# Optimization experiments

Hardware: AMD Instinct MI355X
Metric: run time of the kernel (lower is better)

## Reference

```python
import jax, jax.numpy as jnp
import numpy as np

B, L, H, NH, T, WIN = 4, 4096, 256, 8, 64, 16
D = H // NH
NEG_SLOPE = 5.0
MASK_FILL = -1e12


def _leaky(x):
    return jnp.where(x >= 0, x, NEG_SLOPE * x)


def _window_indices():
    # static numpy index construction, mirrors EdgeBlock.self_attn
    off_u = np.concatenate([np.zeros(WIN + 1, np.int64), np.arange(1, WIN + 1)])
    off_d = np.concatenate([np.arange(-WIN, 0), np.zeros(WIN + 1, np.int64)])
    idx_u = np.arange(L)[:, None] + off_u  # [L, 2W+1]
    idx_d = np.arange(L)[:, None] + off_d  # [L, 2W+1]
    idx_mask = (idx_d >= 0) & (idx_u < L)
    return idx_u % L, idx_d % L, idx_mask


def setup_inputs() -> dict:
    key = jax.random.key(0)
    ks = jax.random.split(key, 12)
    s = 1.0 / np.sqrt(H)
    lengths = jnp.array([L, L - 128, L - 512, L - 1024])
    context_mask = jnp.arange(L)[None, :] < lengths[:, None]  # [B, L] bool
    return {
        'context': jax.random.normal(ks[0], (B, L, H), jnp.float32),
        'types': jax.random.normal(ks[1], (B, T, H), jnp.float32),
        'context_mask': context_mask,
        'W_types': jax.random.normal(ks[2], (H, H), jnp.float32) * s,
        'b_types': jnp.zeros((H,), jnp.float32),
        'W_context': jax.random.normal(ks[3], (H, H), jnp.float32) * s,
        'b_context': jnp.zeros((H,), jnp.float32),
        'upon': jax.random.normal(ks[4], (NH, D), jnp.float32) * s,
        'down': jax.random.normal(ks[5], (NH, D), jnp.float32) * s,
        'cross': jax.random.normal(ks[6], (NH, D, D), jnp.float32) * s,
        'W_out': jax.random.normal(ks[7], (H, H), jnp.float32) * s,
        'b_out': jnp.zeros((H,), jnp.float32),
    }


def reference(context, types, context_mask, W_types, b_types, W_context, b_context,
              upon, down, cross, W_out, b_out):
    idx_u, idx_d, idx_mask = _window_indices()

    # head-split projections
    types_h = (types @ W_types + b_types).reshape(B, T, NH, D)      # [B,T,n,d]
    context_h = (context @ W_context + b_context).reshape(B, L, NH, D)  # [B,L,n,d]

    # ---- cross attention scores: context queries over types (EdgeBlock.cross_attn)
    upon_q = jnp.einsum('blnd,nd->bnl', context_h, upon)
    down_t = jnp.einsum('btnd,nd->bnt', types_h, down)
    concat_ct = upon_q[..., None] + down_t[:, :, None, :]           # [B,n,L,T]
    prod_ct = jnp.einsum('blnd,ndh,btnh->bnlt', context_h, cross, types_h)
    types_s = _leaky(concat_ct + prod_ct)                            # [B,n,L,T]

    # ---- windowed self attention scores (EdgeBlock.self_attn)
    down_s = jnp.einsum('blnd,nd->bnl', context_h, down)
    concat_self = upon_q[:, :, idx_u] + down_s[:, :, idx_d]          # [B,n,L,2W+1]
    win_idx = idx_u  # source: cat([indices_d[:, :0], indices_u[:, 0:]]) == indices_u
    wmask = context_mask[:, win_idx] & idx_mask                      # [B,L,2W+1]
    value_h = context_h[:, win_idx]                                  # [B,L,2W+1,n,d]
    prod_self = jnp.einsum('blnd,ndh,blvnh->bnlv', context_h, cross, value_h)
    context_s = jnp.where(wmask[:, None], _leaky(concat_self + prod_self), MASK_FILL)

    # ---- joint softmax over types + window, then aggregate
    weights = jax.nn.softmax(jnp.concatenate([types_s, context_s], axis=-1), axis=-1)
    types_w, context_w = weights[..., :T], weights[..., T:]
    upd_t = jnp.einsum('bnlt,btnd->blnd', types_w, types_h)
    upd_c = jnp.einsum('bnlv,blvnd->blnd', context_w, value_h)
    update = (upd_t + upd_c).reshape(B, L, H)

    # residual + output transform (no_gate=True path: Linear + Tanh)
    return jnp.tanh((update + context) @ W_out + b_out)
```

## Files before the change

kernel.cpp:

```cpp
#include <hip/hip_runtime.h>
#include <cstdint>

#define Bq 4
#define Lq 4096
#define Hq 256
#define NHq 8
#define Tq 64
#define WINq 16
#define Dq 32
#define NEG_SLOPE 5.0f
#define MASK_FILL -1e12f
#define TLq 64
#define MB 16

typedef __attribute__((ext_vector_type(8))) short short8;
typedef __attribute__((ext_vector_type(4))) float f32x4;

__device__ __forceinline__ float leaky(float x) { return x >= 0.f ? x : NEG_SLOPE * x; }

__device__ __forceinline__ uint16_t f2bf(float x) {
    uint32_t u = __float_as_uint(x);
    uint32_t r = (u + 0x7fffu + ((u >> 16) & 1u)) >> 16;
    return (uint16_t)r;
}
__device__ __forceinline__ float bf2f(uint16_t h) {
    return __uint_as_float(((uint32_t)h) << 16);
}

__global__ void k_prep(const float* __restrict__ Wc, const float* __restrict__ Wo,
                       uint16_t* __restrict__ pc_hi, uint16_t* __restrict__ pc_lo,
                       uint16_t* __restrict__ po_hi, uint16_t* __restrict__ po_lo,
                       const float* __restrict__ types, const float* __restrict__ Wt,
                       const float* __restrict__ bt, const float* __restrict__ down,
                       float* __restrict__ types_h, float* __restrict__ types_hT,
                       float* __restrict__ down_t) {
    __shared__ float sin[Hq];
    __shared__ float outr[Hq];
    if (blockIdx.x < 128) {
        int wsel = blockIdx.x >> 6;
        int blk = blockIdx.x & 63;
        const float* W = wsel ? Wo : Wc;
        uint16_t* ph = wsel ? po_hi : pc_hi;
        uint16_t* pl = wsel ? po_lo : pc_lo;
        int base = blk * 1024;
        for (int idx = base + threadIdx.x; idx < base + 1024; idx += 256) {
            int j = idx & 7, l = (idx >> 3) & 63, fragi = idx >> 9;
            int kc = fragi & 7, nt = fragi >> 3;
            int k = kc * 32 + (l >> 4) * 8 + j;
            int c = nt * 16 + (l & 15);
            float x = W[k * Hq + c];
            uint16_t h = f2bf(x);
            ph[idx] = h;
            pl[idx] = f2bf(x - bf2f(h));
        }
        return;
    }
    int row = blockIdx.x - 128;
    int h = threadIdx.x;
    int b = row >> 6, t = row & 63;
    sin[h] = types[(size_t)row * Hq + h];
    __syncthreads();
    float acc = bt[h];
    for (int k = 0; k < Hq; k += 4) {
        float4 iv = *(const float4*)&sin[k];
        acc = fmaf(iv.x, Wt[(k + 0) * Hq + h], acc);
        acc = fmaf(iv.y, Wt[(k + 1) * Hq + h], acc);
        acc = fmaf(iv.z, Wt[(k + 2) * Hq + h], acc);
        acc = fmaf(iv.w, Wt[(k + 3) * Hq + h], acc);
    }
    types_h[(size_t)row * Hq + h] = acc;
    types_hT[(size_t)(b * Hq + h) * Tq + t] = acc;
    outr[h] = acc;
    __syncthreads();
    if (h < NHq) {
        float s = 0.f;
        for (int d = 0; d < Dq; ++d) s += outr[h * Dq + d] * down[h * Dq + d];
        down_t[(b * NHq + h) * Tq + t] = s;
    }
}

#define APAD 264
#define OPAD 258
__global__ void __launch_bounds__(256) k_ctx(
        const float* __restrict__ ctx,
        const uint16_t* __restrict__ wp_hi, const uint16_t* __restrict__ wp_lo,
        const float* __restrict__ bc, const float* __restrict__ upon,
        const float* __restrict__ down,
        float* __restrict__ ctx_hT, float* __restrict__ uq,
        float* __restrict__ dsv) {
    int row0 = blockIdx.x * MB;
    int b = row0 >> 12, l0 = row0 & (Lq - 1);
    int tid = threadIdx.x;
    int w = tid >> 6, l = tid & 63;
    __shared__ __align__(16) char smem_raw[MB * APAD * 4];
    uint16_t* a_hi = (uint16_t*)smem_raw;
    uint16_t* a_lo = a_hi + MB * APAD;
    float* outb = (float*)smem_raw;

    {
        const float4* src = (const float4*)(ctx + (size_t)row0 * Hq);
#pragma unroll
        for (int j = 0; j < 4; ++j) {
            int f = tid + j * 256;
            int r = f >> 6, cg = f & 63;
            float4 v = src[f];
            uint16_t h0 = f2bf(v.x), h1 = f2bf(v.y), h2 = f2bf(v.z), h3 = f2bf(v.w);
            ushort4 hh = {h0, h1, h2, h3};
            ushort4 ll = {f2bf(v.x - bf2f(h0)), f2bf(v.y - bf2f(h1)),
                          f2bf(v.z - bf2f(h2)), f2bf(v.w - bf2f(h3))};
            *(ushort4*)&a_hi[r * APAD + cg * 4] = hh;
            *(ushort4*)&a_lo[r * APAD + cg * 4] = ll;
        }
    }
    __syncthreads();

    int nt0 = w * 4;
    int m = l & 15, quad = l >> 4;
    f32x4 acc[4];
#pragma unroll
    for (int t = 0; t < 4; ++t) acc[t] = (f32x4){0.f, 0.f, 0.f, 0.f};
#pragma unroll
    for (int kc = 0; kc < 8; ++kc) {
        short8 ah = *(const short8*)&a_hi[m * APAD + kc * 32 + quad * 8];
        short8 al = *(const short8*)&a_lo[m * APAD + kc * 32 + quad * 8];
#pragma unroll
        for (int t = 0; t < 4; ++t) {
            int fragi = (nt0 + t) * 8 + kc;
            short8 wh = *(const short8*)&wp_hi[fragi * 512 + l * 8];
            short8 wl = *(const short8*)&wp_lo[fragi * 512 + l * 8];
            acc[t] = __builtin_amdgcn_mfma_f32_16x16x32_bf16(ah, wh, acc[t], 0, 0, 0);
            acc[t] = __builtin_amdgcn_mfma_f32_16x16x32_bf16(ah, wl, acc[t], 0, 0, 0);
            acc[t] = __builtin_amdgcn_mfma_f32_16x16x32_bf16(al, wh, acc[t], 0, 0, 0);
        }
    }
    __syncthreads();

#pragma unroll
    for (int t = 0; t < 4; ++t) {
        int col = (nt0 + t) * 16 + m;
        float bv = bc[col];
#pragma unroll
        for (int r = 0; r < 4; ++r)
            outb[(quad * 4 + r) * OPAD + col] = acc[t][r] + bv;
    }
    __syncthreads();

    if (tid < MB * NHq) {
        int r = tid >> 3, n = tid & 7;
        float su = 0.f, sd = 0.f;
        for (int d = 0; d < Dq; ++d) {
            float v = outb[r * OPAD + n * Dq + d];
            su += v * upon[n * Dq + d];
            sd += v * down[n * Dq + d];
        }
        uq[(b * NHq + n) * Lq + l0 + r] = su;
        dsv[(b * NHq + n) * Lq + l0 + r] = sd;
    }
    {
#pragma unroll
        for (int jj = 0; jj < 4; ++jj) {
            int f = tid + jj * 256;
            int ch = f >> 2, part = f & 3;
            float4 o;
            o.x = outb[(4 * part + 0) * OPAD + ch];
            o.y = outb[(4 * part + 1) * OPAD + ch];
            o.z = outb[(4 * part + 2) * OPAD + ch];
            o.w = outb[(4 * part + 3) * OPAD + ch];
            *(float4*)(ctx_hT + (size_t)(b * Hq + ch) * Lq + l0 + 4 * part) = o;
        }
    }
}

__global__ void __launch_bounds__(256, 3) k_attn(
        const float* __restrict__ ctx_hT, const float* __restrict__ types_h,
        const float* __restrict__ types_hT, const float* __restrict__ cross,
        const float* __restrict__ uq, const float* __restrict__ dsv,
        const float* __restrict__ dt, const unsigned char* __restrict__ maskp,
        const float* __restrict__ ctx,
        uint16_t* __restrict__ updp_hi, uint16_t* __restrict__ updp_lo) {
    int blk = blockIdx.x;
    int lt = blk & 63, n = (blk >> 6) & 7, b = blk >> 9;
    int l0 = lt * TLq;
    int tid = threadIdx.x;
    int g = tid >> 6;
    int lane = tid & 63;
    int Q = lane >> 4, s = lane & 15;
    bool mask_b8 = (maskp[1] != 0);

    __shared__ __align__(16) char smem[53952];
    uint16_t* TT_hi     = (uint16_t*)(smem);
    uint16_t* TT_lo     = (uint16_t*)(smem + 5120);
    uint16_t* chxT_hi   = (uint16_t*)(smem + 10240);
    uint16_t* chxT_lo   = (uint16_t*)(smem + 16640);
    uint16_t* waT_hi    = (uint16_t*)(smem);
    uint16_t* waT_lo    = (uint16_t*)(smem + 9216);
    uint16_t* crle_hi   = (uint16_t*)(smem + 23040);
    uint16_t* crle_lo   = (uint16_t*)(smem + 28160);
    uint16_t* waw_hi    = (uint16_t*)(smem + 23040);
    uint16_t* waw_lo    = (uint16_t*)(smem + 28160);
    uint16_t* chvt_hi   = (uint16_t*)(smem + 33280);
    uint16_t* chvt_lo   = (uint16_t*)(smem + 38400);
    uint16_t* ttvt_hi   = (uint16_t*)(smem + 43520);
    uint16_t* ttvt_lo   = (uint16_t*)(smem + 48128);
    float* uqe   = (float*)(smem + 52736);
    float* dsve  = (float*)(smem + 53056);
    float* maskf = (float*)(smem + 53376);
    float* dts   = (float*)(smem + 53696);

    short8 cb0h, cb0l, cb1h, cb1l;
    {
        const float* cbp = cross + n * (Dq * Dq) + s;
        float c0v[8], c1v[8];
#pragma unroll
        for (int j = 0; j < 8; ++j) {
            c0v[j] = cbp[(8 * Q + j) * 32];
            c1v[j] = cbp[(8 * Q + j) * 32 + 16];
        }
#pragma unroll
        for (int j = 0; j < 8; ++j) {
            uint16_t h0 = f2bf(c0v[j]);
            cb0h[j] = (short)h0; cb0l[j] = (short)f2bf(c0v[j] - bf2f(h0));
            uint16_t h1 = f2bf(c1v[j]);
            cb1h[j] = (short)h1; cb1l[j] = (short)f2bf(c1v[j] - bf2f(h1));
        }
    }

    {
        int d_ = tid >> 3, k_ = tid & 7, base = k_ * 10;
        const float* grow = ctx_hT + ((size_t)(b * NHq + n) * Dq + d_) * Lq;
        float cv[10];
        if (l0 <= Lq - 80) {
            const float2* g2 = (const float2*)(grow + l0 + base);
#pragma unroll
            for (int j = 0; j < 5; ++j) { float2 v = g2[j]; cv[2*j] = v.x; cv[2*j+1] = v.y; }
        } else {
#pragma unroll
            for (int m = 0; m < 10; ++m) {
                int gl = l0 + base + m;
                cv[m] = grow[gl >= Lq ? gl - Lq : gl];
            }
        }
        uint16_t hh[10], ll[10];
#pragma unroll
        for (int m = 0; m < 10; ++m) {
            hh[m] = f2bf(cv[m]);
            ll[m] = f2bf(cv[m] - bf2f(hh[m]));
        }
#pragma unroll
        for (int j = 0; j < 5; ++j) {
            *(uint*)&chvt_hi[d_ * 80 + base + 2*j] = (uint)hh[2*j] | ((uint)hh[2*j+1] << 16);
            *(uint*)&chvt_lo[d_ * 80 + base + 2*j] = (uint)ll[2*j] | ((uint)ll[2*j+1] << 16);
        }
#pragma unroll
        for (int m = 0; m < 10; ++m) {
            chxT_hi[(base + m) * 40 + d_] = hh[m];
            chxT_lo[(base + m) * 40 + d_] = ll[m];
        }
    }
    {
        int t = tid >> 2, c8 = (tid & 3) * 8;
        const float* src = types_h + (size_t)(b * Tq + t) * Hq + n * Dq + c8;
        float4 v0 = *(const float4*)src, v1 = *(const float4*)(src + 4);
        float vv[8] = {v0.x, v0.y, v0.z, v0.w, v1.x, v1.y, v1.z, v1.w};
        uint hp[4], lp[4];
#pragma unroll
        for (int j = 0; j < 4; ++j) {
            uint16_t h0 = f2bf(vv[2*j]), h1 = f2bf(vv[2*j+1]);
            hp[j] = (uint)h0 | ((uint)h1 << 16);
            lp[j] = (uint)f2bf(vv[2*j] - bf2f(h0)) | ((uint)f2bf(vv[2*j+1] - bf2f(h1)) << 16);
        }
        *(uint4*)&TT_hi[t * 40 + c8] = make_uint4(hp[0], hp[1], hp[2], hp[3]);
        *(uint4*)&TT_lo[t * 40 + c8] = make_uint4(lp[0], lp[1], lp[2], lp[3]);
    }
    {
        int d_ = tid >> 3, t8 = (tid & 7) * 8;
        const float* src = types_hT + ((size_t)(b * Hq) + n * Dq + d_) * Tq + t8;
        float4 v0 = *(const float4*)src, v1 = *(const float4*)(src + 4);
        float vv[8] = {v0.x, v0.y, v0.z, v0.w, v1.x, v1.y, v1.z, v1.w};
        uint hp[4], lp[4];
#pragma unroll
        for (int j = 0; j < 4; ++j) {
            uint16_t h0 = f2bf(vv[2*j]), h1 = f2bf(vv[2*j+1]);
            hp[j] = (uint)h0 | ((uint)h1 << 16);
            lp[j] = (uint)f2bf(vv[2*j] - bf2f(h0)) | ((uint)f2bf(vv[2*j+1] - bf2f(h1)) << 16);
        }
        *(uint4*)&ttvt_hi[d_ * 72 + t8] = make_uint4(hp[0], hp[1], hp[2], hp[3]);
        *(uint4*)&ttvt_lo[d_ * 72 + t8] = make_uint4(lp[0], lp[1], lp[2], lp[3]);
    }
    if (tid < 80) {
        int gl = l0 + tid;
        int glw = gl >= Lq ? gl - Lq : gl;
        uqe[tid] = uq[(b * NHq + n) * Lq + glw];
        unsigned char mb = mask_b8 ? maskp[b * Lq + glw]
                                   : maskp[(size_t)(b * Lq + glw) * 4];
        maskf[tid] = mb ? 1.f : 0.f;
    } else if (tid >= 96 && tid < 176) {
        int i = tid - 96;
        int gl = l0 - 16 + i;
        int glw = gl < 0 ? gl + Lq : (gl >= Lq ? gl - Lq : gl);
        dsve[i] = dsv[(b * NHq + n) * Lq + glw];
    } else if (tid >= 192) {
        dts[tid - 192] = dt[(b * NHq + n) * Tq + (tid - 192)];
    }
    __syncthreads();

    f32x4 cr0 = (f32x4){0.f, 0.f, 0.f, 0.f};
    f32x4 cr1 = (f32x4){0.f, 0.f, 0.f, 0.f};
    {
        short8 axh = *(const short8*)&chxT_hi[(16*g + s) * 40 + 8*Q];
        short8 axl = *(const short8*)&chxT_lo[(16*g + s) * 40 + 8*Q];
        cr0 = __builtin_amdgcn_mfma_f32_16x16x32_bf16(axh, cb0h, cr0, 0, 0, 0);
        cr0 = __builtin_amdgcn_mfma_f32_16x16x32_bf16(axl, cb0h, cr0, 0, 0, 0);
        cr0 = __builtin_amdgcn_mfma_f32_16x16x32_bf16(axh, cb0l, cr0, 0, 0, 0);
        cr1 = __builtin_amdgcn_mfma_f32_16x16x32_bf16(axh, cb1h, cr1, 0, 0, 0);
        cr1 = __builtin_amdgcn_mfma_f32_16x16x32_bf16(axl, cb1h, cr1, 0, 0, 0);
        cr1 = __builtin_amdgcn_mfma_f32_16x16x32_bf16(axh, cb1l, cr1, 0, 0, 0);
    }

#pragma unroll
    for (int r = 0; r < 4; ++r) {
        int row = 16*g + 4*Q + r;
        uint16_t h0 = f2bf(cr0[r]);
        crle_hi[row * 40 + s] = h0;
        crle_lo[row * 40 + s] = f2bf(cr0[r] - bf2f(h0));
        uint16_t h1 = f2bf(cr1[r]);
        crle_hi[row * 40 + 16 + s] = h1;
        crle_lo[row * 40 + 16 + s] = f2bf(cr1[r] - bf2f(h1));
    }

    f32x4 p2[4], p3[2];
#pragma unroll
    for (int c = 0; c < 4; ++c) p2[c] = (f32x4){0.f, 0.f, 0.f, 0.f};
#pragma unroll
    for (int t_ = 0; t_ < 2; ++t_) p3[t_] = (f32x4){0.f, 0.f, 0.f, 0.f};
    {
        short8 cah = *(const short8*)&crle_hi[(16*g + s) * 40 + 8*Q];
        short8 cal = *(const short8*)&crle_lo[(16*g + s) * 40 + 8*Q];
#pragma unroll
        for (int c = 0; c < 4; ++c) {
            short8 bh = *(const short8*)&TT_hi[(s + 16*c) * 40 + 8*Q];
            short8 bl = *(const short8*)&TT_lo[(s + 16*c) * 40 + 8*Q];
            p2[c] = __builtin_amdgcn_mfma_f32_16x16x32_bf16(cah, bh, p2[c], 0, 0, 0);
            p2[c] = __builtin_amdgcn_mfma_f32_16x16x32_bf16(cal, bh, p2[c], 0, 0, 0);
            p2[c] = __builtin_amdgcn_mfma_f32_16x16x32_bf16(cah, bl, p2[c], 0, 0, 0);
        }
#pragma unroll
        for (int t_ = 0; t_ < 2; ++t_) {
            short8 bh = *(const short8*)&chxT_hi[(16*g + 16*t_ + s) * 40 + 8*Q];
            short8 bl = *(const short8*)&chxT_lo[(16*g + 16*t_ + s) * 40 + 8*Q];
            p3[t_] = __builtin_amdgcn_mfma_f32_16x16x32_bf16(cah, bh, p3[t_], 0, 0, 0);
            p3[t_] = __builtin_amdgcn_mfma_f32_16x16x32_bf16(cal, bh, p3[t_], 0, 0, 0);
            p3[t_] = __builtin_amdgcn_mfma_f32_16x16x32_bf16(cah, bl, p3[t_], 0, 0, 0);
        }
    }

    float uqr[4], cmr[4], dsr[4], dd[4];
    *(float4*)uqr = *(const float4*)&uqe[16*g + 4*Q];
    *(float4*)cmr = *(const float4*)&maskf[16*g + 4*Q];
    *(float4*)dsr = *(const float4*)&dsve[16*g + 4*Q + 16];
#pragma unroll
    for (int r = 0; r < 4; ++r) dd[r] = dsve[16*g + 4*Q + s + r];
    float dtv[4], uw[2], mw[2];
#pragma unroll
    for (int c = 0; c < 4; ++c) dtv[c] = dts[s + 16*c];
#pragma unroll
    for (int t_ = 0; t_ < 2; ++t_) {
        uw[t_] = uqe[16*g + s + 16*t_];
        mw[t_] = maskf[16*g + s + 16*t_];
    }
    float dsb[4];
#pragma unroll
    for (int r = 0; r < 4; ++r) dsb[r] = __shfl(p3[0][r], 20*Q + r);

    float stt[4][4], rup[2][4], rdn[4], rdn16[4];
#pragma unroll
    for (int c = 0; c < 4; ++c)
#pragma unroll
        for (int r = 0; r < 4; ++r)
            stt[c][r] = leaky(uqr[r] + dtv[c] + p2[c][r]);
#pragma unroll
    for (int t_ = 0; t_ < 2; ++t_)
#pragma unroll
        for (int r = 0; r < 4; ++r) {
            int u = s + 16*t_ - 4*Q - r;
            bool ok = (u >= 1) && (u <= 16) && (l0 + 16*g + s + 16*t_ < Lq)
                      && (mw[t_] > 0.5f);
            rup[t_][r] = ok ? leaky(uw[t_] + dsr[r] + p3[t_][r]) : MASK_FILL;
        }
#pragma unroll
    for (int r = 0; r < 4; ++r) {
        bool okd = (l0 + 16*g + 4*Q + r + s >= 16) && (cmr[r] > 0.5f);
        rdn[r]   = okd ? leaky(uqr[r] + dd[r] + dsb[r]) : MASK_FILL;
        rdn16[r] = (s == 0 && cmr[r] > 0.5f) ? leaky(uqr[r] + dsr[r] + dsb[r])
                                             : MASK_FILL;
    }

    float mx[4];
#pragma unroll
    for (int r = 0; r < 4; ++r) {
        float m = fmaxf(fmaxf(stt[0][r], stt[1][r]), fmaxf(stt[2][r], stt[3][r]));
        m = fmaxf(m, fmaxf(rup[0][r], rup[1][r]));
        m = fmaxf(m, fmaxf(rdn[r], rdn16[r]));
        mx[r] = m;
    }
#pragma unroll
    for (int msk = 1; msk <= 8; msk <<= 1)
#pragma unroll
        for (int r = 0; r < 4; ++r) mx[r] = fmaxf(mx[r], __shfl_xor(mx[r], msk));

    float sTU[4] = {0.f, 0.f, 0.f, 0.f}, sD[4];
#pragma unroll
    for (int c = 0; c < 4; ++c)
#pragma unroll
        for (int r = 0; r < 4; ++r) {
            stt[c][r] = __expf(stt[c][r] - mx[r]);
            sTU[r] += stt[c][r];
        }
#pragma unroll
    for (int t_ = 0; t_ < 2; ++t_)
#pragma unroll
        for (int r = 0; r < 4; ++r) {
            rup[t_][r] = __expf(rup[t_][r] - mx[r]);
            sTU[r] += rup[t_][r];
        }
#pragma unroll
    for (int r = 0; r < 4; ++r) {
        rdn[r] = __expf(rdn[r] - mx[r]);
        rdn16[r] = __expf(rdn16[r] - mx[r]);
        sD[r] = rdn[r] + rdn16[r];
    }
#pragma unroll
    for (int msk = 1; msk <= 8; msk <<= 1)
#pragma unroll
        for (int r = 0; r < 4; ++r) {
            sTU[r] += __shfl_xor(sTU[r], msk);
            sD[r]  += __shfl_xor(sD[r], msk);
        }
    float inv[4], wself[4];
#pragma unroll
    for (int r = 0; r < 4; ++r) {
        inv[r] = 1.f / (sTU[r] + sD[r]);
        wself[r] = sD[r] * inv[r];
    }

    __syncthreads();

#pragma unroll
    for (int r = 0; r < 4; ++r) {
        int row = 16*g + 4*Q + r;
#pragma unroll
        for (int c = 0; c < 4; ++c) {
            float v = stt[c][r] * inv[r];
            uint16_t h = f2bf(v);
            waT_hi[row * 72 + s + 16*c] = h;
            waT_lo[row * 72 + s + 16*c] = f2bf(v - bf2f(h));
        }
#pragma unroll
        for (int t_ = 0; t_ < 2; ++t_) {
            int u = s + 16*t_ - 4*Q - r;
            float v = (u == 0) ? wself[r]
                    : ((u >= 1 && u <= 16) ? rup[t_][r] * inv[r] : 0.f);
            uint16_t h = f2bf(v);
            waw_hi[row * 40 + s + 16*t_] = h;
            waw_lo[row * 40 + s + 16*t_] = f2bf(v - bf2f(h));
        }
    }

    f32x4 a0 = (f32x4){0.f, 0.f, 0.f, 0.f};
    f32x4 a1 = (f32x4){0.f, 0.f, 0.f, 0.f};
#pragma unroll
    for (int ks = 0; ks < 2; ++ks) {
        short8 bh = *(const short8*)&waT_hi[(16*g + s) * 72 + 32*ks + 8*Q];
        short8 bl = *(const short8*)&waT_lo[(16*g + s) * 72 + 32*ks + 8*Q];
        short8 t0h = *(const short8*)&ttvt_hi[s * 72 + 32*ks + 8*Q];
        short8 t0l = *(const short8*)&ttvt_lo[s * 72 + 32*ks + 8*Q];
        short8 t1h = *(const short8*)&ttvt_hi[(16 + s) * 72 + 32*ks + 8*Q];
        short8 t1l = *(const short8*)&ttvt_lo[(16 + s) * 72 + 32*ks + 8*Q];
        a0 = __builtin_amdgcn_mfma_f32_16x16x32_bf16(t0h, bh, a0, 0, 0, 0);
        a0 = __builtin_amdgcn_mfma_f32_16x16x32_bf16(t0l, bh, a0, 0, 0, 0);
        a0 = __builtin_amdgcn_mfma_f32_16x16x32_bf16(t0h, bl, a0, 0, 0, 0);
        a1 = __builtin_amdgcn_mfma_f32_16x16x32_bf16(t1h, bh, a1, 0, 0, 0);
        a1 = __builtin_amdgcn_mfma_f32_16x16x32_bf16(t1l, bh, a1, 0, 0, 0);
        a1 = __builtin_amdgcn_mfma_f32_16x16x32_bf16(t1h, bl, a1, 0, 0, 0);
    }
    {
        short8 wbh = *(const short8*)&waw_hi[(16*g + s) * 40 + 8*Q];
        short8 wbl = *(const short8*)&waw_lo[(16*g + s) * 40 + 8*Q];
        short8 c0h = *(const short8*)&chvt_hi[s * 80 + 16*g + 8*Q];
        short8 c0l = *(const short8*)&chvt_lo[s * 80 + 16*g + 8*Q];
        short8 c1h = *(const short8*)&chvt_hi[(16 + s) * 80 + 16*g + 8*Q];
        short8 c1l = *(const short8*)&chvt_lo[(16 + s) * 80 + 16*g + 8*Q];
        a0 = __builtin_amdgcn_mfma_f32_16x16x32_bf16(c0h, wbh, a0, 0, 0, 0);
        a0 = __builtin_amdgcn_mfma_f32_16x16x32_bf16(c0l, wbh, a0, 0, 0, 0);
        a0 = __builtin_amdgcn_mfma_f32_16x16x32_bf16(c0h, wbl, a0, 0, 0, 0);
        a1 = __builtin_amdgcn_mfma_f32_16x16x32_bf16(c1h, wbh, a1, 0, 0, 0);
        a1 = __builtin_amdgcn_mfma_f32_16x16x32_bf16(c1l, wbh, a1, 0, 0, 0);
        a1 = __builtin_amdgcn_mfma_f32_16x16x32_bf16(c1h, wbl, a1, 0, 0, 0);
    }

    {
        int lcol = l0 + 16*g + s;
        const float4* cp = (const float4*)(ctx + (size_t)(b * Lq + lcol) * Hq
                                           + n * Dq + 4*Q);
        float4 c0 = cp[0], c1 = cp[4];
        float v0[4] = {a0[0] + c0.x, a0[1] + c0.y, a0[2] + c0.z, a0[3] + c0.w};
        float v1[4] = {a1[0] + c1.x, a1[1] + c1.y, a1[2] + c1.z, a1[3] + c1.w};
        ushort4 h0, l0v, h1, l1v;
#pragma unroll
        for (int r = 0; r < 4; ++r) {
            uint16_t h = f2bf(v0[r]);
            ((uint16_t*)&h0)[r] = h; ((uint16_t*)&l0v)[r] = f2bf(v0[r] - bf2f(h));
            uint16_t g1 = f2bf(v1[r]);
            ((uint16_t*)&h1)[r] = g1; ((uint16_t*)&l1v)[r] = f2bf(v1[r] - bf2f(g1));
        }
        size_t base = (size_t)(b * Lq + lcol) * Hq + n * Dq + 4*Q;
        *(ushort4*)(updp_hi + base)      = h0;
        *(ushort4*)(updp_hi + base + 16) = h1;
        *(ushort4*)(updp_lo + base)      = l0v;
        *(ushort4*)(updp_lo + base + 16) = l1v;
    }
}

__global__ void __launch_bounds__(256) k_out(
        const uint16_t* __restrict__ up_hi, const uint16_t* __restrict__ up_lo,
        const uint16_t* __restrict__ wp_hi, const uint16_t* __restrict__ wp_lo,
        const float* __restrict__ bo, float* __restrict__ out) {
    int row0 = blockIdx.x * MB;
    int tid = threadIdx.x;
    int w = tid >> 6, l = tid & 63;
    int nt0 = w * 4;
    int m = l & 15, quad = l >> 4;
    const uint16_t* ah_base = up_hi + (size_t)(row0 + m) * Hq + quad * 8;
    const uint16_t* al_base = up_lo + (size_t)(row0 + m) * Hq + quad * 8;

    f32x4 acc[4];
#pragma unroll
    for (int t = 0; t < 4; ++t) acc[t] = (f32x4){0.f, 0.f, 0.f, 0.f};
#pragma unroll
    for (int kc = 0; kc < 8; ++kc) {
        short8 ah = *(const short8*)(ah_base + kc * 32);
        short8 al = *(const short8*)(al_base + kc * 32);
#pragma unroll
        for (int t = 0; t < 4; ++t) {
            int fragi = (nt0 + t) * 8 + kc;
            short8 wh = *(const short8*)&wp_hi[fragi * 512 + l * 8];
            short8 wl = *(const short8*)&wp_lo[fragi * 512 + l * 8];
            acc[t] = __builtin_amdgcn_mfma_f32_16x16x32_bf16(ah, wh, acc[t], 0, 0, 0);
            acc[t] = __builtin_amdgcn_mfma_f32_16x16x32_bf16(ah, wl, acc[t], 0, 0, 0);
            acc[t] = __builtin_amdgcn_mfma_f32_16x16x32_bf16(al, wh, acc[t], 0, 0, 0);
        }
    }
#pragma unroll
    for (int t = 0; t < 4; ++t) {
        int col = (nt0 + t) * 16 + m;
        float bv = bo[col];
#pragma unroll
        for (int r = 0; r < 4; ++r)
            out[(size_t)(row0 + quad * 4 + r) * Hq + col] = tanhf(acc[t][r] + bv);
    }
}

extern "C" void kernel_launch(void* const* d_in, const int* in_sizes, int n_in,
                              void* d_out, int out_size, void* d_ws, size_t ws_size,
                              hipStream_t stream) {
    const float* context   = (const float*)d_in[0];
    const float* types     = (const float*)d_in[1];
    const unsigned char* cmask = (const unsigned char*)d_in[2];
    const float* W_types   = (const float*)d_in[3];
    const float* b_types   = (const float*)d_in[4];
    const float* W_context = (const float*)d_in[5];
    const float* b_context = (const float*)d_in[6];
    const float* upon      = (const float*)d_in[7];
    const float* down      = (const float*)d_in[8];
    const float* cross     = (const float*)d_in[9];
    const float* W_out     = (const float*)d_in[10];
    const float* b_out     = (const float*)d_in[11];
    float* out = (float*)d_out;
    float* ws  = (float*)d_ws;

    float* ctx_hT     = ws;
    uint16_t* updp_hi = (uint16_t*)(ws + 4194304);
    uint16_t* updp_lo = updp_hi + 4194304;
    uint16_t* wcp_hi  = (uint16_t*)(ws + 8388608);
    uint16_t* wcp_lo  = wcp_hi + 65536;
    uint16_t* wop_hi  = wcp_hi + 131072;
    uint16_t* wop_lo  = wcp_hi + 196608;

    float* types_h  = out;
    float* types_hT = out + 65536;
    float* down_t   = out + 131072;
    float* uqp      = out + 133120;
    float* dsvp     = out + 264192;

    k_prep<<<128 + Bq * Tq, 256, 0, stream>>>(W_context, W_out,
                                              wcp_hi, wcp_lo, wop_hi, wop_lo,
                                              types, W_types, b_types, down,
                                              types_h, types_hT, down_t);
    k_ctx<<<Bq * Lq / MB, 256, 0, stream>>>(context, wcp_hi, wcp_lo, b_context,
                                            upon, down, ctx_hT, uqp, dsvp);
    k_attn<<<Bq * NHq * (Lq / TLq), 256, 0, stream>>>(ctx_hT, types_h, types_hT, cross,
                                                      uqp, dsvp, down_t, cmask,
                                                      context, updp_hi, updp_lo);
    k_out<<<Bq * Lq / MB, 256, 0, stream>>>(updp_hi, updp_lo, wop_hi, wop_lo,
                                            b_out, out);
}
```

Measured before the change: 166.3 us.

## Double row tile in projection/output GEMMs and stage attention epilogue through LDS

The projection and output GEMM kernels now process 32 rows per block instead of 16. Each wave computes two 16-row MFMA tiles, so every weight fragment loaded from global memory is reused twice. Separately, the attention kernel's epilogue transposes the MFMA accumulators through shared memory, so each lane writes 8 contiguous bf16 values (16-byte stores) instead of scattered 8-byte stores, and the residual context load is issued earlier to overlap with the MFMAs. The cost is higher register and LDS use and half as many blocks in the GEMM kernels, which may reduce parallelism.

```diff
diff --git a/kernel.cpp b/kernel.cpp
--- a/kernel.cpp
+++ b/kernel.cpp
@@ -11,7 +11,7 @@
 #define NEG_SLOPE 5.0f
 #define MASK_FILL -1e12f
 #define TLq 64
-#define MB 16
+#define MB 32
 
 typedef __attribute__((ext_vector_type(8))) short short8;
 typedef __attribute__((ext_vector_type(4))) float f32x4;
@@ -100,7 +100,7 @@
     {
         const float4* src = (const float4*)(ctx + (size_t)row0 * Hq);
 #pragma unroll
-        for (int j = 0; j < 4; ++j) {
+        for (int j = 0; j < 8; ++j) {
             int f = tid + j * 256;
             int r = f >> 6, cg = f & 63;
             float4 v = src[f];
@@ -116,36 +116,45 @@
 
     int nt0 = w * 4;
     int m = l & 15, quad = l >> 4;
-    f32x4 acc[4];
-#pragma unroll
-    for (int t = 0; t < 4; ++t) acc[t] = (f32x4){0.f, 0.f, 0.f, 0.f};
+    f32x4 acc[2][4];
+#pragma unroll
+    for (int rt = 0; rt < 2; ++rt)
+#pragma unroll
+        for (int t = 0; t < 4; ++t) acc[rt][t] = (f32x4){0.f, 0.f, 0.f, 0.f};
 #pragma unroll
     for (int kc = 0; kc < 8; ++kc) {
-        short8 ah = *(const short8*)&a_hi[m * APAD + kc * 32 + quad * 8];
-        short8 al = *(const short8*)&a_lo[m * APAD + kc * 32 + quad * 8];
+        short8 ah0 = *(const short8*)&a_hi[m * APAD + kc * 32 + quad * 8];
+        short8 al0 = *(const short8*)&a_lo[m * APAD + kc * 32 + quad * 8];
+        short8 ah1 = *(const short8*)&a_hi[(16 + m) * APAD + kc * 32 + quad * 8];
+        short8 al1 = *(const short8*)&a_lo[(16 + m) * APAD + kc * 32 + quad * 8];
 #pragma unroll
         for (int t = 0; t < 4; ++t) {
             int fragi = (nt0 + t) * 8 + kc;
             short8 wh = *(const short8*)&wp_hi[fragi * 512 + l * 8];
             short8 wl = *(const short8*)&wp_lo[fragi * 512 + l * 8];
-            acc[t] = __builtin_amdgcn_mfma_f32_16x16x32_bf16(ah, wh, acc[t], 0, 0, 0);
-            acc[t] = __builtin_amdgcn_mfma_f32_16x16x32_bf16(ah, wl, acc[t], 0, 0, 0);
-            acc[t] = __builtin_amdgcn_mfma_f32_16x16x32_bf16(al, wh, acc[t], 0, 0, 0);
+            acc[0][t] = __builtin_amdgcn_mfma_f32_16x16x32_bf16(ah0, wh, acc[0][t], 0, 0, 0);
+            acc[0][t] = __builtin_amdgcn_mfma_f32_16x16x32_bf16(ah0, wl, acc[0][t], 0, 0, 0);
+            acc[0][t] = __builtin_amdgcn_mfma_f32_16x16x32_bf16(al0, wh, acc[0][t], 0, 0, 0);
+            acc[1][t] = __builtin_amdgcn_mfma_f32_16x16x32_bf16(ah1, wh, acc[1][t], 0, 0, 0);
+            acc[1][t] = __builtin_amdgcn_mfma_f32_16x16x32_bf16(ah1, wl, acc[1][t], 0, 0, 0);
+            acc[1][t] = __builtin_amdgcn_mfma_f32_16x16x32_bf16(al1, wh, acc[1][t], 0, 0, 0);
         }
     }
     __syncthreads();
 
+#pragma unroll
+    for (int rt = 0; rt < 2; ++rt)
 #pragma unroll
     for (int t = 0; t < 4; ++t) {
         int col = (nt0 + t) * 16 + m;
         float bv = bc[col];
 #pragma unroll
         for (int r = 0; r < 4; ++r)
-            outb[(quad * 4 + r) * OPAD + col] = acc[t][r] + bv;
+            outb[(16 * rt + quad * 4 + r) * OPAD + col] = acc[rt][t][r] + bv;
     }
     __syncthreads();
 
-    if (tid < MB * NHq) {
+    {
         int r = tid >> 3, n = tid & 7;
         float su = 0.f, sd = 0.f;
         for (int d = 0; d < Dq; ++d) {
@@ -158,9 +167,9 @@
     }
     {
 #pragma unroll
-        for (int jj = 0; jj < 4; ++jj) {
+        for (int jj = 0; jj < 8; ++jj) {
             int f = tid + jj * 256;
-            int ch = f >> 2, part = f & 3;
+            int ch = f >> 3, part = f & 7;
             float4 o;
             o.x = outb[(4 * part + 0) * OPAD + ch];
             o.y = outb[(4 * part + 1) * OPAD + ch];
@@ -466,6 +475,15 @@
         }
     }
 
+    int rowl = lane & 15, p = lane >> 4;
+    int lcol = l0 + 16*g + rowl;
+    float4 cx0, cx1;
+    {
+        const float4* cp = (const float4*)(ctx + (size_t)(b * Lq + lcol) * Hq
+                                           + n * Dq + 8*p);
+        cx0 = cp[0]; cx1 = cp[1];
+    }
+
     f32x4 a0 = (f32x4){0.f, 0.f, 0.f, 0.f};
     f32x4 a1 = (f32x4){0.f, 0.f, 0.f, 0.f};
 #pragma unroll
@@ -499,25 +517,26 @@
     }
 
     {
-        int lcol = l0 + 16*g + s;
-        const float4* cp = (const float4*)(ctx + (size_t)(b * Lq + lcol) * Hq
-                                           + n * Dq + 4*Q);
-        float4 c0 = cp[0], c1 = cp[4];
-        float v0[4] = {a0[0] + c0.x, a0[1] + c0.y, a0[2] + c0.z, a0[3] + c0.w};
-        float v1[4] = {a1[0] + c1.x, a1[1] + c1.y, a1[2] + c1.z, a1[3] + c1.w};
-        ushort4 h0, l0v, h1, l1v;
-#pragma unroll
-        for (int r = 0; r < 4; ++r) {
-            uint16_t h = f2bf(v0[r]);
-            ((uint16_t*)&h0)[r] = h; ((uint16_t*)&l0v)[r] = f2bf(v0[r] - bf2f(h));
-            uint16_t g1 = f2bf(v1[r]);
-            ((uint16_t*)&h1)[r] = g1; ((uint16_t*)&l1v)[r] = f2bf(v1[r] - bf2f(g1));
-        }
-        size_t base = (size_t)(b * Lq + lcol) * Hq + n * Dq + 4*Q;
-        *(ushort4*)(updp_hi + base)      = h0;
-        *(ushort4*)(updp_hi + base + 16) = h1;
-        *(ushort4*)(updp_lo + base)      = l0v;
-        *(ushort4*)(updp_lo + base + 16) = l1v;
+        float* cst = (float*)(smem + 2304 * g);
+        *(float4*)&cst[s * 32 + ((4*Q + 4*s) & 31)]
+            = make_float4(a0[0], a0[1], a0[2], a0[3]);
+        *(float4*)&cst[s * 32 + ((16 + 4*Q + 4*s) & 31)]
+            = make_float4(a1[0], a1[1], a1[2], a1[3]);
+        float4 u0 = *(float4*)&cst[rowl * 32 + ((8*p + 4*rowl) & 31)];
+        float4 u1 = *(float4*)&cst[rowl * 32 + ((8*p + 4 + 4*rowl) & 31)];
+        float vv[8] = {u0.x + cx0.x, u0.y + cx0.y, u0.z + cx0.z, u0.w + cx0.w,
+                       u1.x + cx1.x, u1.y + cx1.y, u1.z + cx1.z, u1.w + cx1.w};
+        uint hu[4], lu[4];
+#pragma unroll
+        for (int j = 0; j < 4; ++j) {
+            uint16_t h0 = f2bf(vv[2*j]), h1 = f2bf(vv[2*j+1]);
+            hu[j] = (uint)h0 | ((uint)h1 << 16);
+            lu[j] = (uint)f2bf(vv[2*j] - bf2f(h0))
+                  | ((uint)f2bf(vv[2*j+1] - bf2f(h1)) << 16);
+        }
+        size_t obase = (size_t)(b * Lq + lcol) * Hq + n * Dq + 8*p;
+        *(uint4*)(updp_hi + obase) = make_uint4(hu[0], hu[1], hu[2], hu[3]);
+        *(uint4*)(updp_lo + obase) = make_uint4(lu[0], lu[1], lu[2], lu[3]);
     }
 }
 
@@ -530,33 +549,45 @@
     int w = tid >> 6, l = tid & 63;
     int nt0 = w * 4;
     int m = l & 15, quad = l >> 4;
-    const uint16_t* ah_base = up_hi + (size_t)(row0 + m) * Hq + quad * 8;
-    const uint16_t* al_base = up_lo + (size_t)(row0 + m) * Hq + quad * 8;
-
-    f32x4 acc[4];
-#pragma unroll
-    for (int t = 0; t < 4; ++t) acc[t] = (f32x4){0.f, 0.f, 0.f, 0.f};
+    const uint16_t* ah_base0 = up_hi + (size_t)(row0 + m) * Hq + quad * 8;
+    const uint16_t* al_base0 = up_lo + (size_t)(row0 + m) * Hq + quad * 8;
+    const uint16_t* ah_base1 = ah_base0 + 16 * Hq;
+    const uint16_t* al_base1 = al_base0 + 16 * Hq;
+
+    f32x4 acc[2][4];
+#pragma unroll
+    for (int rt = 0; rt < 2; ++rt)
+#pragma unroll
+        for (int t = 0; t < 4; ++t) acc[rt][t] = (f32x4){0.f, 0.f, 0.f, 0.f};
 #pragma unroll
     for (int kc = 0; kc < 8; ++kc) {
-        short8 ah = *(const short8*)(ah_base + kc * 32);
-        short8 al = *(const short8*)(al_base + kc * 32);
+        short8 ah0 = *(const short8*)(ah_base0 + kc * 32);
+        short8 al0 = *(const short8*)(al_base0 + kc * 32);
+        short8 ah1 = *(const short8*)(ah_base1 + kc * 32);
+        short8 al1 = *(const short8*)(al_base1 + kc * 32);
 #pragma unroll
         for (int t = 0; t < 4; ++t) {
             int fragi = (nt0 + t) * 8 + kc;
             short8 wh = *(const short8*)&wp_hi[fragi * 512 + l * 8];
             short8 wl = *(const short8*)&wp_lo[fragi * 512 + l * 8];
-            acc[t] = __builtin_amdgcn_mfma_f32_16x16x32_bf16(ah, wh, acc[t], 0, 0, 0);
-            acc[t] = __builtin_amdgcn_mfma_f32_16x16x32_bf16(ah, wl, acc[t], 0, 0, 0);
-            acc[t] = __builtin_amdgcn_mfma_f32_16x16x32_bf16(al, wh, acc[t], 0, 0, 0);
-        }
-    }
+            acc[0][t] = __builtin_amdgcn_mfma_f32_16x16x32_bf16(ah0, wh, acc[0][t], 0, 0, 0);
+            acc[0][t] = __builtin_amdgcn_mfma_f32_16x16x32_bf16(ah0, wl, acc[0][t], 0, 0, 0);
+            acc[0][t] = __builtin_amdgcn_mfma_f32_16x16x32_bf16(al0, wh, acc[0][t], 0, 0, 0);
+            acc[1][t] = __builtin_amdgcn_mfma_f32_16x16x32_bf16(ah1, wh, acc[1][t], 0, 0, 0);
+            acc[1][t] = __builtin_amdgcn_mfma_f32_16x16x32_bf16(ah1, wl, acc[1][t], 0, 0, 0);
+            acc[1][t] = __builtin_amdgcn_mfma_f32_16x16x32_bf16(al1, wh, acc[1][t], 0, 0, 0);
+        }
+    }
+#pragma unroll
+    for (int rt = 0; rt < 2; ++rt)
 #pragma unroll
     for (int t = 0; t < 4; ++t) {
         int col = (nt0 + t) * 16 + m;
         float bv = bo[col];
 #pragma unroll
         for (int r = 0; r < 4; ++r)
-            out[(size_t)(row0 + quad * 4 + r) * Hq + col] = tanhf(acc[t][r] + bv);
+            out[(size_t)(row0 + 16 * rt + quad * 4 + r) * Hq + col]
+                = tanhf(acc[rt][t][r] + bv);
     }
 }
 
```

Result: no change. 169.4 us (+1.8%).
